# Kernel tuning notes

Hardware: AMD Instinct MI355X
Metric: run time of the kernel (lower is better)

## Reference

```python
import jax, jax.numpy as jnp
import numpy as np
from jax import lax

EPS = 1e-5  # torch BatchNorm2d default


def setup_inputs() -> dict:
    key = jax.random.key(0)
    k1, k2, k3 = jax.random.split(key, 3)
    C = 64
    x = jax.random.normal(k1, (32, C, 128, 128), dtype=jnp.float32)
    # per-channel 3x3 depthwise weights (OIHW with I=1, feature_group_count=C)
    w = jax.random.normal(k2, (C, 1, 3, 3), dtype=jnp.float32) * (1.0 / 3.0)
    b = jax.random.normal(k3, (C,), dtype=jnp.float32) * 0.1
    gamma = jnp.ones((C,), dtype=jnp.float32)
    beta = jnp.zeros((C,), dtype=jnp.float32)
    return {"x": x, "w": w, "b": b, "gamma": gamma, "beta": beta}


def reference(x, w, b, gamma, beta):
    C = x.shape[1]
    # depthwise 3x3 conv, stride 1, padding 1 (same math as C separate Conv2d(1,1,3))
    y = lax.conv_general_dilated(
        x, w,
        window_strides=(1, 1),
        padding=((1, 1), (1, 1)),
        feature_group_count=C,
        dimension_numbers=("NCHW", "OIHW", "NCHW"),
    )
    y = y + b[None, :, None, None]
    # BatchNorm2d(1) per channel in training mode: batch stats over (N, H, W),
    # biased variance, eps=1e-5
    mean = jnp.mean(y, axis=(0, 2, 3), keepdims=True)
    var = jnp.var(y, axis=(0, 2, 3), keepdims=True)
    y_hat = (y - mean) * lax.rsqrt(var + EPS)
    out = y_hat * gamma[None, :, None, None] + beta[None, :, None, None]
    return jax.nn.relu(out)
```

## Files before the change

### kernel.cpp

```cpp
#include <hip/hip_runtime.h>

#define HW        128
#define PLANE     16384
#define NCH       64
#define NB        32
#define NPLANES   2048
#define COUNT_INV (1.0f / 524288.0f)
#define EPSV      1e-5f


__device__ __forceinline__ void load_row(const float* __restrict__ bp, int g, int w4,
                                         bool hasL, bool hasR, float (&v)[6]) {
    if ((unsigned)g < (unsigned)HW) {
        const float* rp = bp + g * HW + w4;
        float4 m = *(const float4*)rp;
        v[0] = hasL ? rp[-1] : 0.f;
        v[1] = m.x; v[2] = m.y; v[3] = m.z; v[4] = m.w;
        v[5] = hasR ? rp[4] : 0.f;
    } else {
        v[0] = 0.f; v[1] = 0.f; v[2] = 0.f; v[3] = 0.f; v[4] = 0.f; v[5] = 0.f;
    }
}

__device__ __forceinline__ void conv_row(const float (&tp)[6], const float (&md)[6],
                                         const float (&bt)[6], const float* W,
                                         float bias, float (&acc)[4]) {
#pragma unroll
    for (int j = 0; j < 4; ++j) {
        float a = bias;
        a = fmaf(tp[j],     W[0], a);
        a = fmaf(tp[j + 1], W[1], a);
        a = fmaf(tp[j + 2], W[2], a);
        a = fmaf(md[j],     W[3], a);
        a = fmaf(md[j + 1], W[4], a);
        a = fmaf(md[j + 2], W[5], a);
        a = fmaf(bt[j],     W[6], a);
        a = fmaf(bt[j + 1], W[7], a);
        a = fmaf(bt[j + 2], W[8], a);
        acc[j] = a;
    }
}

__global__ __launch_bounds__(256, 4) void pass_stats(const float* __restrict__ x,
                                                     const float* __restrict__ wgt,
                                                     const float* __restrict__ bias,
                                                     float* __restrict__ partials) {
    __shared__ float red[8];
    const int p  = blockIdx.x;
    const int c  = p & 63;
    const int t  = threadIdx.x;
    const int cg = t & 31, rg = t >> 5;
    const int w4 = cg * 4, r0 = rg * 16;

    float W[9];
#pragma unroll
    for (int k = 0; k < 9; ++k) W[k] = wgt[c * 9 + k];
    const float bv = bias[c];
    const float* bp = x + (size_t)p * PLANE;
    const bool hasL = (cg != 0), hasR = (cg != 31);

    float v[3][6];
    load_row(bp, r0 - 1, w4, hasL, hasR, v[0]);
    load_row(bp, r0,     w4, hasL, hasR, v[1]);

    float sum = 0.f, sq = 0.f;
#pragma unroll
    for (int i = 0; i < 16; ++i) {
        load_row(bp, r0 + 1 + i, w4, hasL, hasR, v[(i + 2) % 3]);
        float acc[4];
        conv_row(v[i % 3], v[(i + 1) % 3], v[(i + 2) % 3], W, bv, acc);
#pragma unroll
        for (int j = 0; j < 4; ++j) {
            sum += acc[j];
            sq = fmaf(acc[j], acc[j], sq);
        }
    }

#pragma unroll
    for (int off = 32; off; off >>= 1) {
        sum += __shfl_down(sum, off);
        sq  += __shfl_down(sq, off);
    }
    const int wave = t >> 6, lane = t & 63;
    if (lane == 0) { red[wave] = sum; red[4 + wave] = sq; }
    __syncthreads();
    if (t == 0) {
        partials[p]           = red[0] + red[1] + red[2] + red[3];
        partials[NPLANES + p] = red[4] + red[5] + red[6] + red[7];
    }
}

__global__ __launch_bounds__(256, 4) void pass_apply(const float* __restrict__ x,
                                                     const float* __restrict__ wgt,
                                                     const float* __restrict__ bias,
                                                     const float* __restrict__ partials,
                                                     const float* __restrict__ gamma,
                                                     const float* __restrict__ beta,
                                                     float* __restrict__ out) {
    __shared__ float ssh[2];
    const int p  = blockIdx.x;
    const int c  = p & 63;
    const int t  = threadIdx.x;
    const int cg = t & 31, rg = t >> 5;
    const int w4 = cg * 4, r0 = rg * 16;

    if (t < 32) {
        float S = partials[t * NCH + c];
        float Q = partials[NPLANES + t * NCH + c];
#pragma unroll
        for (int off = 16; off; off >>= 1) {
            S += __shfl_down(S, off);
            Q += __shfl_down(Q, off);
        }
        if (t == 0) {
            float mean = S * COUNT_INV;
            float var  = fmaxf(Q * COUNT_INV - mean * mean, 0.f);
            float s    = gamma[c] * rsqrtf(var + EPSV);
            ssh[0] = s;
            ssh[1] = beta[c] - mean * s;
        }
    }

    float W[9];
#pragma unroll
    for (int k = 0; k < 9; ++k) W[k] = wgt[c * 9 + k];
    const float bv = bias[c];
    __syncthreads();
    const float s  = ssh[0];
    const float sh = fmaf(bv, s, ssh[1]);

    const float* bp = x + (size_t)p * PLANE;
    float* op = out + (size_t)p * PLANE;
    const bool hasL = (cg != 0), hasR = (cg != 31);

    float v[3][6];
    load_row(bp, r0 - 1, w4, hasL, hasR, v[0]);
    load_row(bp, r0,     w4, hasL, hasR, v[1]);

#pragma unroll
    for (int i = 0; i < 16; ++i) {
        load_row(bp, r0 + 1 + i, w4, hasL, hasR, v[(i + 2) % 3]);
        float acc[4];
        conv_row(v[i % 3], v[(i + 1) % 3], v[(i + 2) % 3], W, 0.f, acc);
        float4 o;
        o.x = fmaxf(fmaf(acc[0], s, sh), 0.f);
        o.y = fmaxf(fmaf(acc[1], s, sh), 0.f);
        o.z = fmaxf(fmaf(acc[2], s, sh), 0.f);
        o.w = fmaxf(fmaf(acc[3], s, sh), 0.f);
        *(float4*)(op + (r0 + i) * HW + w4) = o;
    }
}

extern "C" void kernel_launch(void* const* d_in, const int* in_sizes, int n_in,
                              void* d_out, int out_size, void* d_ws, size_t ws_size,
                              hipStream_t stream) {
    const float* x     = (const float*)d_in[0];
    const float* w     = (const float*)d_in[1];
    const float* b     = (const float*)d_in[2];
    const float* gamma = (const float*)d_in[3];
    const float* beta  = (const float*)d_in[4];
    float* out = (float*)d_out;
    float* ws  = (float*)d_ws;

    pass_stats<<<NPLANES, 256, 0, stream>>>(x, w, b, ws);
    pass_apply<<<NPLANES, 256, 0, stream>>>(x, w, b, ws, gamma, beta, out);
}
```

Before: 79.17 us.

## Fuse stats and apply passes into one cooperative kernel with grid sync

Replaces the two-kernel stats/apply pipeline with a single cooperative kernel of 1024 blocks, each handling two planes of one channel. After computing per-plane partial sums, blocks synchronize across the grid, compute BN scale/shift, then recompute the convolution and write output. Planes are revisited in reverse order so the most recently read one is more likely still in L2/LLC, which cuts re-read DRAM traffic and removes one launch. The cost is a grid-wide barrier, reliance on all 1024 blocks being co-resident (4 per CU), and a fallback to the old path if occupancy is insufficient.

Measured after the change: 78.82 us. Within noise of the previous version (-0.5%).

```diff
diff --git a/kernel.cpp b/kernel.cpp
--- a/kernel.cpp
+++ b/kernel.cpp
@@ -1,4 +1,7 @@
 #include <hip/hip_runtime.h>
+#include <hip/hip_cooperative_groups.h>
+
+namespace cg = cooperative_groups;
 
 #define HW        128
 #define PLANE     16384
@@ -7,6 +10,7 @@
 #define NPLANES   2048
 #define COUNT_INV (1.0f / 524288.0f)
 #define EPSV      1e-5f
+#define GRID_F    1024
 
 
 __device__ __forceinline__ void load_row(const float* __restrict__ bp, int g, int w4,
@@ -41,6 +45,119 @@
     }
 }
 
+__device__ __forceinline__ void plane_sums(const float* __restrict__ bp, int r0, int w4,
+                                           bool hasL, bool hasR, const float* W,
+                                           float bv, float& sum, float& sq) {
+    float v[3][6];
+    load_row(bp, r0 - 1, w4, hasL, hasR, v[0]);
+    load_row(bp, r0,     w4, hasL, hasR, v[1]);
+    sum = 0.f; sq = 0.f;
+#pragma unroll
+    for (int i = 0; i < 16; ++i) {
+        load_row(bp, r0 + 1 + i, w4, hasL, hasR, v[(i + 2) % 3]);
+        float acc[4];
+        conv_row(v[i % 3], v[(i + 1) % 3], v[(i + 2) % 3], W, bv, acc);
+#pragma unroll
+        for (int j = 0; j < 4; ++j) {
+            sum += acc[j];
+            sq = fmaf(acc[j], acc[j], sq);
+        }
+    }
+}
+
+__device__ __forceinline__ void plane_store(const float* __restrict__ bp,
+                                            float* __restrict__ op, int r0, int w4,
+                                            bool hasL, bool hasR, const float* W,
+                                            float s, float sh) {
+    float v[3][6];
+    load_row(bp, r0 - 1, w4, hasL, hasR, v[0]);
+    load_row(bp, r0,     w4, hasL, hasR, v[1]);
+#pragma unroll
+    for (int i = 0; i < 16; ++i) {
+        load_row(bp, r0 + 1 + i, w4, hasL, hasR, v[(i + 2) % 3]);
+        float acc[4];
+        conv_row(v[i % 3], v[(i + 1) % 3], v[(i + 2) % 3], W, 0.f, acc);
+        float4 o;
+        o.x = fmaxf(fmaf(acc[0], s, sh), 0.f);
+        o.y = fmaxf(fmaf(acc[1], s, sh), 0.f);
+        o.z = fmaxf(fmaf(acc[2], s, sh), 0.f);
+        o.w = fmaxf(fmaf(acc[3], s, sh), 0.f);
+        *(float4*)(op + (r0 + i) * HW + w4) = o;
+    }
+}
+
+__global__ __launch_bounds__(256, 4) void fused(const float* __restrict__ x,
+                                                const float* __restrict__ wgt,
+                                                const float* __restrict__ bias,
+                                                const float* __restrict__ gamma,
+                                                const float* __restrict__ beta,
+                                                float* __restrict__ partials,
+                                                float* __restrict__ out) {
+    __shared__ float red[8];
+    __shared__ float ssh[2];
+    const int bid = blockIdx.x;
+    const int c   = bid & 63;
+    const int np  = bid >> 6;
+    const int t   = threadIdx.x;
+    const int cg_ = t & 31, rg = t >> 5;
+    const int w4  = cg_ * 4, r0 = rg * 16;
+    const bool hasL = (cg_ != 0), hasR = (cg_ != 31);
+
+    float W[9];
+#pragma unroll
+    for (int k = 0; k < 9; ++k) W[k] = wgt[c * 9 + k];
+    const float bv = bias[c];
+
+    for (int pp = 0; pp < 2; ++pp) {
+        const int p = (np * 2 + pp) * NCH + c;
+        const float* bp = x + (size_t)p * PLANE;
+        float sum, sq;
+        plane_sums(bp, r0, w4, hasL, hasR, W, bv, sum, sq);
+#pragma unroll
+        for (int off = 32; off; off >>= 1) {
+            sum += __shfl_down(sum, off);
+            sq  += __shfl_down(sq, off);
+        }
+        const int wave = t >> 6, lane = t & 63;
+        if (lane == 0) { red[wave] = sum; red[4 + wave] = sq; }
+        __syncthreads();
+        if (t == 0) {
+            partials[p]           = red[0] + red[1] + red[2] + red[3];
+            partials[NPLANES + p] = red[4] + red[5] + red[6] + red[7];
+        }
+        __syncthreads();
+    }
+    __threadfence();
+    cg::this_grid().sync();
+
+    if (t < 32) {
+        float S = partials[t * NCH + c];
+        float Q = partials[NPLANES + t * NCH + c];
+#pragma unroll
+        for (int off = 16; off; off >>= 1) {
+            S += __shfl_down(S, off);
+            Q += __shfl_down(Q, off);
+        }
+        if (t == 0) {
+            float mean = S * COUNT_INV;
+            float var  = fmaxf(Q * COUNT_INV - mean * mean, 0.f);
+            float s    = gamma[c] * rsqrtf(var + EPSV);
+            ssh[0] = s;
+            ssh[1] = beta[c] - mean * s;
+        }
+    }
+    __syncthreads();
+    const float s  = ssh[0];
+    const float sh = fmaf(bv, s, ssh[1]);
+
+    for (int pp = 1; pp >= 0; --pp) {
+        const int p = (np * 2 + pp) * NCH + c;
+        const float* bp = x + (size_t)p * PLANE;
+        float* op = out + (size_t)p * PLANE;
+        plane_store(bp, op, r0, w4, hasL, hasR, W, s, sh);
+    }
+}
+
 __global__ __launch_bounds__(256, 4) void pass_stats(const float* __restrict__ x,
                                                      const float* __restrict__ wgt,
                                                      const float* __restrict__ bias,
@@ -49,33 +166,18 @@
     const int p  = blockIdx.x;
     const int c  = p & 63;
     const int t  = threadIdx.x;
-    const int cg = t & 31, rg = t >> 5;
-    const int w4 = cg * 4, r0 = rg * 16;
+    const int cg_ = t & 31, rg = t >> 5;
+    const int w4 = cg_ * 4, r0 = rg * 16;
+    const bool hasL = (cg_ != 0), hasR = (cg_ != 31);
 
     float W[9];
 #pragma unroll
     for (int k = 0; k < 9; ++k) W[k] = wgt[c * 9 + k];
     const float bv = bias[c];
     const float* bp = x + (size_t)p * PLANE;
-    const bool hasL = (cg != 0), hasR = (cg != 31);
-
-    float v[3][6];
-    load_row(bp, r0 - 1, w4, hasL, hasR, v[0]);
-    load_row(bp, r0,     w4, hasL, hasR, v[1]);
-
-    float sum = 0.f, sq = 0.f;
-#pragma unroll
-    for (int i = 0; i < 16; ++i) {
-        load_row(bp, r0 + 1 + i, w4, hasL, hasR, v[(i + 2) % 3]);
-        float acc[4];
-        conv_row(v[i % 3], v[(i + 1) % 3], v[(i + 2) % 3], W, bv, acc);
-#pragma unroll
-        for (int j = 0; j < 4; ++j) {
-            sum += acc[j];
-            sq = fmaf(acc[j], acc[j], sq);
-        }
-    }
-
+
+    float sum, sq;
+    plane_sums(bp, r0, w4, hasL, hasR, W, bv, sum, sq);
 #pragma unroll
     for (int off = 32; off; off >>= 1) {
         sum += __shfl_down(sum, off);
@@ -101,8 +203,9 @@
     const int p  = blockIdx.x;
     const int c  = p & 63;
     const int t  = threadIdx.x;
-    const int cg = t & 31, rg = t >> 5;
-    const int w4 = cg * 4, r0 = rg * 16;
+    const int cg_ = t & 31, rg = t >> 5;
+    const int w4 = cg_ * 4, r0 = rg * 16;
+    const bool hasL = (cg_ != 0), hasR = (cg_ != 31);
 
     if (t < 32) {
         float S = partials[t * NCH + c];
@@ -131,24 +234,7 @@
 
     const float* bp = x + (size_t)p * PLANE;
     float* op = out + (size_t)p * PLANE;
-    const bool hasL = (cg != 0), hasR = (cg != 31);
-
-    float v[3][6];
-    load_row(bp, r0 - 1, w4, hasL, hasR, v[0]);
-    load_row(bp, r0,     w4, hasL, hasR, v[1]);
-
-#pragma unroll
-    for (int i = 0; i < 16; ++i) {
-        load_row(bp, r0 + 1 + i, w4, hasL, hasR, v[(i + 2) % 3]);
-        float acc[4];
-        conv_row(v[i % 3], v[(i + 1) % 3], v[(i + 2) % 3], W, 0.f, acc);
-        float4 o;
-        o.x = fmaxf(fmaf(acc[0], s, sh), 0.f);
-        o.y = fmaxf(fmaf(acc[1], s, sh), 0.f);
-        o.z = fmaxf(fmaf(acc[2], s, sh), 0.f);
-        o.w = fmaxf(fmaf(acc[3], s, sh), 0.f);
-        *(float4*)(op + (r0 + i) * HW + w4) = o;
-    }
+    plane_store(bp, op, r0, w4, hasL, hasR, W, s, sh);
 }
 
 extern "C" void kernel_launch(void* const* d_in, const int* in_sizes, int n_in,
@@ -162,6 +248,19 @@
     float* out = (float*)d_out;
     float* ws  = (float*)d_ws;
 
-    pass_stats<<<NPLANES, 256, 0, stream>>>(x, w, b, ws);
-    pass_apply<<<NPLANES, 256, 0, stream>>>(x, w, b, ws, gamma, beta, out);
-}
+    int nb = 0;
+    hipError_t qe = hipOccupancyMaxActiveBlocksPerMultiprocessor(
+        &nb, reinterpret_cast<const void*>(fused), 256, 0);
+
+    if (qe == hipSuccess && nb >= 4) {
+        const float* xa = x; const float* wa = w; const float* ba = b;
+        const float* ga = gamma; const float* be = beta;
+        float* pw = ws; float* oa = out;
+        void* args[] = {&xa, &wa, &ba, &ga, &be, &pw, &oa};
+        hipLaunchCooperativeKernel(reinterpret_cast<const void*>(fused),
+                                   dim3(GRID_F), dim3(256), args, 0, stream);
+    } else {
+        pass_stats<<<NPLANES, 256, 0, stream>>>(x, w, b, ws);
+        pass_apply<<<NPLANES, 256, 0, stream>>>(x, w, b, ws, gamma, beta, out);
+    }
+}
```

## Split each plane into four blocks with preloaded 6-row windows and nontemporal stores

Applied to the files above, without the earlier changes.

Each plane is now handled by four blocks, and each thread computes 4 output rows instead of 16. All six input rows are loaded up front, which gives more memory-level parallelism, and the halo re-read overhead rises to 6/4 rows. The channel reduction in the apply pass is now done by a full wave over 128 partials laid out contiguously per channel, which removes the shared-memory sync and lets the statistics load overlap the input loads. Output stores use nontemporal hints so they avoid polluting the cache.

Result: faster. 75.02 us (-5.2%).

```diff
diff --git a/kernel.cpp b/kernel.cpp
--- a/kernel.cpp
+++ b/kernel.cpp
@@ -4,21 +4,29 @@
 #define PLANE     16384
 #define NCH       64
 #define NB        32
-#define NPLANES   2048
+#define NQ        4
+#define NPART     8192
 #define COUNT_INV (1.0f / 524288.0f)
 #define EPSV      1e-5f
 
+typedef float f4v __attribute__((ext_vector_type(4)));
 
-__device__ __forceinline__ void load_row(const float* __restrict__ bp, int g, int w4,
-                                         bool hasL, bool hasR, float (&v)[6]) {
-    if ((unsigned)g < (unsigned)HW) {
-        const float* rp = bp + g * HW + w4;
-        float4 m = *(const float4*)rp;
-        v[0] = hasL ? rp[-1] : 0.f;
-        v[1] = m.x; v[2] = m.y; v[3] = m.z; v[4] = m.w;
-        v[5] = hasR ? rp[4] : 0.f;
-    } else {
-        v[0] = 0.f; v[1] = 0.f; v[2] = 0.f; v[3] = 0.f; v[4] = 0.f; v[5] = 0.f;
+
+__device__ __forceinline__ void load_win(const float* __restrict__ bp, int r0, int w4,
+                                         bool hasL, bool hasR, float (&v)[6][6]) {
+#pragma unroll
+    for (int i = 0; i < 6; ++i) {
+        int g = r0 - 1 + i;
+        if ((unsigned)g < (unsigned)HW) {
+            const float* rp = bp + g * HW + w4;
+            float4 m = *(const float4*)rp;
+            v[i][0] = hasL ? rp[-1] : 0.f;
+            v[i][1] = m.x; v[i][2] = m.y; v[i][3] = m.z; v[i][4] = m.w;
+            v[i][5] = hasR ? rp[4] : 0.f;
+        } else {
+#pragma unroll
+            for (int j = 0; j < 6; ++j) v[i][j] = 0.f;
+        }
     }
 }
 
@@ -41,34 +49,35 @@
     }
 }
 
-__global__ __launch_bounds__(256, 4) void pass_stats(const float* __restrict__ x,
-                                                     const float* __restrict__ wgt,
-                                                     const float* __restrict__ bias,
-                                                     float* __restrict__ partials) {
+__global__ __launch_bounds__(256) void pass_stats(const float* __restrict__ x,
+                                                  const float* __restrict__ wgt,
+                                                  const float* __restrict__ bias,
+                                                  float* __restrict__ partials) {
     __shared__ float red[8];
-    const int p  = blockIdx.x;
-    const int c  = p & 63;
-    const int t  = threadIdx.x;
-    const int cg = t & 31, rg = t >> 5;
-    const int w4 = cg * 4, r0 = rg * 16;
+    const int bid   = blockIdx.x;
+    const int q     = bid & 3;
+    const int plane = bid >> 2;
+    const int c     = plane & 63;
+    const int n     = plane >> 6;
+    const int t     = threadIdx.x;
+    const int cg    = t & 31, rg = t >> 5;
+    const int w4    = cg * 4, r0 = q * 32 + rg * 4;
+    const bool hasL = (cg != 0), hasR = (cg != 31);
 
     float W[9];
 #pragma unroll
     for (int k = 0; k < 9; ++k) W[k] = wgt[c * 9 + k];
     const float bv = bias[c];
-    const float* bp = x + (size_t)p * PLANE;
-    const bool hasL = (cg != 0), hasR = (cg != 31);
+    const float* bp = x + (size_t)plane * PLANE;
 
-    float v[3][6];
-    load_row(bp, r0 - 1, w4, hasL, hasR, v[0]);
-    load_row(bp, r0,     w4, hasL, hasR, v[1]);
+    float v[6][6];
+    load_win(bp, r0, w4, hasL, hasR, v);
 
     float sum = 0.f, sq = 0.f;
 #pragma unroll
-    for (int i = 0; i < 16; ++i) {
-        load_row(bp, r0 + 1 + i, w4, hasL, hasR, v[(i + 2) % 3]);
+    for (int k = 0; k < 4; ++k) {
         float acc[4];
-        conv_row(v[i % 3], v[(i + 1) % 3], v[(i + 2) % 3], W, bv, acc);
+        conv_row(v[k], v[k + 1], v[k + 2], W, bv, acc);
 #pragma unroll
         for (int j = 0; j < 4; ++j) {
             sum += acc[j];
@@ -85,69 +94,61 @@
     if (lane == 0) { red[wave] = sum; red[4 + wave] = sq; }
     __syncthreads();
     if (t == 0) {
-        partials[p]           = red[0] + red[1] + red[2] + red[3];
-        partials[NPLANES + p] = red[4] + red[5] + red[6] + red[7];
+        const int pi = n * 4 + q;
+        partials[c * 128 + pi]         = red[0] + red[1] + red[2] + red[3];
+        partials[NPART + c * 128 + pi] = red[4] + red[5] + red[6] + red[7];
     }
 }
 
-__global__ __launch_bounds__(256, 4) void pass_apply(const float* __restrict__ x,
-                                                     const float* __restrict__ wgt,
-                                                     const float* __restrict__ bias,
-                                                     const float* __restrict__ partials,
-                                                     const float* __restrict__ gamma,
-                                                     const float* __restrict__ beta,
-                                                     float* __restrict__ out) {
-    __shared__ float ssh[2];
-    const int p  = blockIdx.x;
-    const int c  = p & 63;
-    const int t  = threadIdx.x;
-    const int cg = t & 31, rg = t >> 5;
-    const int w4 = cg * 4, r0 = rg * 16;
-
-    if (t < 32) {
-        float S = partials[t * NCH + c];
-        float Q = partials[NPLANES + t * NCH + c];
-#pragma unroll
-        for (int off = 16; off; off >>= 1) {
-            S += __shfl_down(S, off);
-            Q += __shfl_down(Q, off);
-        }
-        if (t == 0) {
-            float mean = S * COUNT_INV;
-            float var  = fmaxf(Q * COUNT_INV - mean * mean, 0.f);
-            float s    = gamma[c] * rsqrtf(var + EPSV);
-            ssh[0] = s;
-            ssh[1] = beta[c] - mean * s;
-        }
-    }
+__global__ __launch_bounds__(256) void pass_apply(const float* __restrict__ x,
+                                                  const float* __restrict__ wgt,
+                                                  const float* __restrict__ bias,
+                                                  const float* __restrict__ partials,
+                                                  const float* __restrict__ gamma,
+                                                  const float* __restrict__ beta,
+                                                  float* __restrict__ out) {
+    const int bid   = blockIdx.x;
+    const int q     = bid & 3;
+    const int plane = bid >> 2;
+    const int c     = plane & 63;
+    const int t     = threadIdx.x;
+    const int cg    = t & 31, rg = t >> 5;
+    const int w4    = cg * 4, r0 = q * 32 + rg * 4;
+    const bool hasL = (cg != 0), hasR = (cg != 31);
 
     float W[9];
 #pragma unroll
     for (int k = 0; k < 9; ++k) W[k] = wgt[c * 9 + k];
     const float bv = bias[c];
-    __syncthreads();
-    const float s  = ssh[0];
-    const float sh = fmaf(bv, s, ssh[1]);
+    const float* bp = x + (size_t)plane * PLANE;
 
-    const float* bp = x + (size_t)p * PLANE;
-    float* op = out + (size_t)p * PLANE;
-    const bool hasL = (cg != 0), hasR = (cg != 31);
+    float v[6][6];
+    load_win(bp, r0, w4, hasL, hasR, v);
 
-    float v[3][6];
-    load_row(bp, r0 - 1, w4, hasL, hasR, v[0]);
-    load_row(bp, r0,     w4, hasL, hasR, v[1]);
+    const int lane = t & 63;
+    float S = partials[c * 128 + lane]         + partials[c * 128 + 64 + lane];
+    float Q = partials[NPART + c * 128 + lane] + partials[NPART + c * 128 + 64 + lane];
+#pragma unroll
+    for (int off = 32; off; off >>= 1) {
+        S += __shfl_xor(S, off);
+        Q += __shfl_xor(Q, off);
+    }
+    const float mean = S * COUNT_INV;
+    const float var  = fmaxf(Q * COUNT_INV - mean * mean, 0.f);
+    const float s    = gamma[c] * rsqrtf(var + EPSV);
+    const float sh   = fmaf(bv, s, beta[c] - mean * s);
 
+    float* op = out + (size_t)plane * PLANE;
 #pragma unroll
-    for (int i = 0; i < 16; ++i) {
-        load_row(bp, r0 + 1 + i, w4, hasL, hasR, v[(i + 2) % 3]);
+    for (int k = 0; k < 4; ++k) {
         float acc[4];
-        conv_row(v[i % 3], v[(i + 1) % 3], v[(i + 2) % 3], W, 0.f, acc);
-        float4 o;
+        conv_row(v[k], v[k + 1], v[k + 2], W, 0.f, acc);
+        f4v o;
         o.x = fmaxf(fmaf(acc[0], s, sh), 0.f);
         o.y = fmaxf(fmaf(acc[1], s, sh), 0.f);
         o.z = fmaxf(fmaf(acc[2], s, sh), 0.f);
         o.w = fmaxf(fmaf(acc[3], s, sh), 0.f);
-        *(float4*)(op + (r0 + i) * HW + w4) = o;
+        __builtin_nontemporal_store(o, (f4v*)(op + (r0 + k) * HW + w4));
     }
 }
 
@@ -162,6 +163,6 @@
     float* out = (float*)d_out;
     float* ws  = (float*)d_ws;
 
-    pass_stats<<<NPLANES, 256, 0, stream>>>(x, w, b, ws);
-    pass_apply<<<NPLANES, 256, 0, stream>>>(x, w, b, ws, gamma, beta, out);
+    pass_stats<<<NB * NCH * NQ, 256, 0, stream>>>(x, w, b, ws);
+    pass_apply<<<NB * NCH * NQ, 256, 0, stream>>>(x, w, b, ws, gamma, beta, out);
 }
```
